# Performance work log

Hardware: AMD Instinct MI355X
Metric: run time of the kernel (lower is better)

## Reference

```python
import jax, jax.numpy as jnp
import numpy as np

DILATIONS_REST = (2, 4, 8, 16, 32, 64)


def _causal_conv(x, v, g, b, dilation):
    # weight-norm: w = g * v / ||v||_(in,k) per out-channel
    norm = jnp.sqrt(jnp.sum(v * v, axis=(1, 2), keepdims=True))
    w = g[:, None, None] * v / norm                      # [O, I, K]
    pad = (v.shape[2] - 1) * dilation                    # left-only causal pad
    y = jax.lax.conv_general_dilated(
        x, w, window_strides=(1,), padding=[(pad, 0)],
        rhs_dilation=(dilation,), dimension_numbers=('NCH', 'OIH', 'NCH'))
    return y + b[None, :, None]


def setup_inputs() -> dict:
    key = jax.random.key(0)
    ks = jax.random.split(key, 16)
    B, T, V, E = 64, 2048, 32000, 300
    inp = {
        'inputs': jax.random.randint(ks[0], (B, T), 0, V),
        'de_feature': jax.random.normal(ks[1], (B, 11), dtype=jnp.float32),
        'emb': jax.random.normal(ks[2], (V, E), dtype=jnp.float32) * 0.02,
        'v0': jax.random.normal(ks[3], (128, 300, 5), dtype=jnp.float32) * 0.05,
        'g0': jnp.ones((128,), dtype=jnp.float32),
        'b0': jax.random.normal(ks[4], (128,), dtype=jnp.float32) * 0.01,
        'vr': jax.random.normal(ks[5], (6, 128, 128, 5), dtype=jnp.float32) * 0.05,
        'gr': jnp.ones((6, 128), dtype=jnp.float32),
        'br': jax.random.normal(ks[6], (6, 128), dtype=jnp.float32) * 0.01,
        'fc1_w': jax.random.normal(ks[7], (64, 139), dtype=jnp.float32) * 0.08,
        'fc1_b': jnp.zeros((64,), dtype=jnp.float32),
        'fc2_w': jax.random.normal(ks[8], (32, 64), dtype=jnp.float32) * 0.12,
        'fc2_b': jnp.zeros((32,), dtype=jnp.float32),
        'fc3_w': jax.random.normal(ks[9], (1, 32), dtype=jnp.float32) * 0.17,
        'fc3_b': jnp.zeros((1,), dtype=jnp.float32),
    }
    return inp


def reference(inputs, de_feature, emb, v0, g0, b0, vr, gr, br,
              fc1_w, fc1_b, fc2_w, fc2_b, fc3_w, fc3_b):
    x = emb[inputs]                       # [B, T, 300]
    x = jnp.transpose(x, (0, 2, 1))       # [B, 300, T]
    x = jax.nn.relu(_causal_conv(x, v0, g0, b0, 1))
    for i, d in enumerate(DILATIONS_REST):
        x = jax.nn.relu(_causal_conv(x, vr[i], gr[i], br[i], d))
    emb_v = x[:, :, -1]                   # last timestep [B, 128]
    combo = jnp.concatenate([emb_v, de_feature], axis=1)  # [B, 139]
    h = jax.nn.relu(combo @ fc1_w.T + fc1_b)
    h = jax.nn.relu(h @ fc2_w.T + fc2_b)
    logits = h @ fc3_w.T + fc3_b          # [B, 1]
    return logits
```

## Files before the change

### kernel.cpp

```cpp
#include <hip/hip_runtime.h>


typedef __attribute__((ext_vector_type(8))) short bfrag8;
typedef __attribute__((ext_vector_type(4))) float floatx4;
typedef __attribute__((ext_vector_type(4))) short short4v;
typedef __attribute__((ext_vector_type(4))) float float4v;

__device__ __forceinline__ unsigned short f2bf(float f) {
  union { float f; unsigned u; } v; v.f = f;
  unsigned r = v.u + 0x7fffu + ((v.u >> 16) & 1u);
  return (unsigned short)(r >> 16);
}
__device__ __forceinline__ float bf2f(unsigned short h) {
  union { unsigned u; float f; } v; v.u = ((unsigned)h) << 16;
  return v.f;
}
__device__ __forceinline__ int swz(int row) { return ((row >> 1) & 7) << 4; }

__global__ __launch_bounds__(512)
void k_prep(const float* __restrict__ v0, const float* __restrict__ g0,
            const float* __restrict__ vr, const float* __restrict__ gr,
            const int* __restrict__ tokens, const float* __restrict__ emb,
            unsigned short* __restrict__ WB0, unsigned short* __restrict__ WBr,
            unsigned short* __restrict__ In0) {
  const int blk = blockIdx.x;
  if (blk >= 112) {
    const int gidx = ((blk - 112) << 9) + threadIdx.x;
    const int TOT = 64 * 520 * 80;
    for (int idx = gidx; idx < TOT; idx += 2560 * 512) {
      const int c8 = idx % 80;
      const int rem = idx / 80;
      const int p = rem % 520;
      const int b = rem / 520;
      short4v o = {0, 0, 0, 0};
      if (p < 509 && c8 < 75) {
        const int tok = tokens[(b << 11) + 1539 + p];
        const float4v v = *(const float4v*)(emb + (size_t)tok * 300 + (c8 << 2));
        o[0] = (short)f2bf(v[0]); o[1] = (short)f2bf(v[1]);
        o[2] = (short)f2bf(v[2]); o[3] = (short)f2bf(v[3]);
      }
      *(short4v*)(In0 + ((size_t)b * 520 + p) * 320 + (c8 << 2)) = o;
    }
    return;
  }
  const int gw = (blk << 3) + (threadIdx.x >> 6);
  const int lane = threadIdx.x & 63;
  if (gw < 128) {
    const int o = gw;
    const float* v = v0 + o * 1500;
    float ss = 0.f;
    for (int i = lane; i < 1500; i += 64) { const float x = v[i]; ss += x * x; }
#pragma unroll
    for (int off = 32; off; off >>= 1) ss += __shfl_xor(ss, off, 64);
    const float scale = g0[o] * rsqrtf(ss);
    const int ot = o >> 4;
    for (int kk = lane; kk < 1600; kk += 64) {
      const int tap = kk / 320, c = kk % 320;
      const float w = (c < 300) ? v[c * 5 + tap] * scale : 0.f;
      const int ks = kk >> 5;
      const int li = (o & 15) | (((kk >> 3) & 3) << 4);
      WB0[(((ot * 50 + ks) * 64 + li) << 3) | (kk & 7)] = f2bf(w);
    }
  } else {
    const int idx = gw - 128;
    const int l = idx >> 7, o = idx & 127;
    const float* v = vr + (size_t)(l * 128 + o) * 640;
    float ss = 0.f;
#pragma unroll
    for (int i = 0; i < 10; ++i) { const float x = v[lane + (i << 6)]; ss += x * x; }
#pragma unroll
    for (int off = 32; off; off >>= 1) ss += __shfl_xor(ss, off, 64);
    const float scale = gr[l * 128 + o] * rsqrtf(ss);
    unsigned short* WB = WBr + (size_t)l * 81920;
    const int ot = o >> 4;
#pragma unroll
    for (int i = 0; i < 10; ++i) {
      const int kk = lane + (i << 6);
      const int tap = kk >> 7, c = kk & 127;
      const float w = v[c * 5 + tap] * scale;
      const int ks = kk >> 5;
      const int li = (o & 15) | (((kk >> 3) & 3) << 4);
      WB[(((ot * 20 + ks) * 64 + li) << 3) | (kk & 7)] = f2bf(w);
    }
  }
}

__global__ __launch_bounds__(512, 1)
void k_conv0(const unsigned short* __restrict__ In0,
             const unsigned short* __restrict__ WB, const float* __restrict__ b0,
             unsigned short* __restrict__ A0) {
  __shared__ char buf[131 * 656];
  const int tid = threadIdx.x;
  const int qt = blockIdx.x, b = blockIdx.y;
  const char* src = (const char*)(In0 + ((size_t)b * 520 + (qt << 7)) * 320);
  for (int idx = tid; idx < 131 * 41; idx += 512) {
    const int r = idx / 41, s = idx - r * 41;
    float4v v = {0.f, 0.f, 0.f, 0.f};
    if (s < 40) v = *(const float4v*)(src + r * 640 + (s << 4));
    *(float4v*)(buf + r * 656 + (s << 4)) = v;
  }
  __syncthreads();
  const int lane = tid & 63, w = tid >> 6;
  const int og = w & 3, mg = w >> 2;
  const int qb = lane & 15, kg = lane >> 4;
  floatx4 acc[2][2];
#pragma unroll
  for (int m = 0; m < 2; ++m) {
    acc[m][0] = floatx4{0.f, 0.f, 0.f, 0.f};
    acc[m][1] = floatx4{0.f, 0.f, 0.f, 0.f};
  }
  const unsigned short* wb0 = WB + (size_t)((((og << 1) * 50) << 6) + lane) * 8;
#pragma unroll
  for (int tap = 0; tap < 5; ++tap) {
    bfrag8 bf0[10], bf1[10];
#pragma unroll
    for (int cs = 0; cs < 10; ++cs) {
      const int ks = tap * 10 + cs;
      bf0[cs] = *(const bfrag8*)(wb0 + (ks << 9));
      bf1[cs] = *(const bfrag8*)(wb0 + ((ks + 50) << 9));
    }
#pragma unroll
    for (int cs = 0; cs < 10; ++cs) {
      const int cb = (cs << 6) + (kg << 4);
#pragma unroll
      for (int m = 0; m < 2; ++m) {
        const int row = (((((mg << 1) + m) << 4) + qb) << 1) + tap;
        const bfrag8 a = *(const bfrag8*)(buf + row * 656 + cb);
        acc[m][0] = __builtin_amdgcn_mfma_f32_16x16x32_bf16(a, bf0[cs], acc[m][0], 0, 0, 0);
        acc[m][1] = __builtin_amdgcn_mfma_f32_16x16x32_bf16(a, bf1[cs], acc[m][1], 0, 0, 0);
      }
    }
  }
  unsigned short* ob = A0 + (((size_t)b << 8) + (qt << 6)) * 128;
  const int o0 = (og << 5) + qb;
  const float bv0 = b0[o0], bv1 = b0[o0 + 16];
#pragma unroll
  for (int m = 0; m < 2; ++m)
#pragma unroll
    for (int r = 0; r < 4; ++r) {
      const int ql = ((((mg << 1) + m) << 4) + (kg << 2)) + r;
      ob[ql * 128 + o0]      = f2bf(fmaxf(acc[m][0][r] + bv0, 0.f));
      ob[ql * 128 + o0 + 16] = f2bf(fmaxf(acc[m][1][r] + bv1, 0.f));
    }
}

template<int NMTW, int NOTW, int MTILES>
__device__ __forceinline__ void conv_rest(const char* bi, char* bo,
    const unsigned short* __restrict__ WBl, const float* __restrict__ bias,
    int w, int qb, int kg, int lane) {
  constexpr int NG = MTILES / NMTW;
  const int mg = (NG == 1) ? 0 : (w % NG);
  const int og = (NG == 1) ? w : (w / NG);
  if (og >= 8 / NOTW) return;
  floatx4 acc[NMTW][NOTW];
#pragma unroll
  for (int m = 0; m < NMTW; ++m)
#pragma unroll
    for (int j = 0; j < NOTW; ++j) acc[m][j] = floatx4{0.f, 0.f, 0.f, 0.f};
#pragma unroll
  for (int quarter = 0; quarter < 4; ++quarter) {
    bfrag8 bfs[NOTW][5];
#pragma unroll
    for (int j = 0; j < NOTW; ++j)
#pragma unroll
      for (int t = 0; t < 5; ++t)
        bfs[j][t] = *(const bfrag8*)(WBl +
            (size_t)(((((og * NOTW + j) * 20) + quarter * 5 + t) << 6) + lane) * 8);
#pragma unroll
    for (int t = 0; t < 5; ++t) {
      const int ks = quarter * 5 + t, tap = ks >> 2, cs = ks & 3;
#pragma unroll
      for (int m = 0; m < NMTW; ++m) {
        const int row = (((((mg * NMTW + m) << 4) + qb)) << 1) + tap;
        const int byte = ((row << 8) + (cs << 6) + (kg << 4)) ^ swz(row);
        const bfrag8 a = *(const bfrag8*)(bi + byte);
#pragma unroll
        for (int j = 0; j < NOTW; ++j)
          acc[m][j] = __builtin_amdgcn_mfma_f32_16x16x32_bf16(a, bfs[j][t], acc[m][j], 0, 0, 0);
      }
    }
  }
#pragma unroll
  for (int m = 0; m < NMTW; ++m)
#pragma unroll
    for (int j = 0; j < NOTW; ++j) {
      const int o = ((og * NOTW + j) << 4) + qb;
      const float bv = bias[o];
#pragma unroll
      for (int r = 0; r < 4; ++r) {
        const int qq = ((mg * NMTW + m) << 4) + (kg << 2) + r;
        const int byte2 = ((qq << 8) + (o << 1)) ^ swz(qq);
        *(unsigned short*)(bo + byte2) = f2bf(fmaxf(acc[m][j][r] + bv, 0.f));
      }
    }
}

__global__ __launch_bounds__(1024, 1)
void k_tail(const unsigned short* __restrict__ A0, const unsigned short* __restrict__ WBr,
            const float* __restrict__ br, const float* __restrict__ de,
            const float* __restrict__ w1, const float* __restrict__ b1,
            const float* __restrict__ w2, const float* __restrict__ b2,
            const float* __restrict__ w3, const float* __restrict__ b3,
            float* __restrict__ out) {
  __shared__ char lds[65024 + 32768 + 16384 + 384 + 2048];
  char* bufIn = lds;
  char* actP  = lds + 65024;
  char* actQ  = lds + 97792;
  float* h1   = (float*)(lds + 114176);
  float* h2   = (float*)(lds + 114432);
  const int tid = threadIdx.x, b = blockIdx.x;
  const int lane = tid & 63, w = tid >> 6;
  const int qb = lane & 15, kg = lane >> 4;

  const char* a0b = (const char*)(A0 + ((size_t)b << 15));
  for (int idx = tid; idx < 253 * 16; idx += 1024) {
    const int r = idx >> 4, s = idx & 15;
    *(float4v*)(bufIn + (((r << 8) + (s << 4)) ^ swz(r))) =
        *(const float4v*)(a0b + (r << 8) + (s << 4));
  }
  __syncthreads();

  conv_rest<2, 2, 8>(bufIn, actP, WBr + 0 * 81920, br + 0,   w, qb, kg, lane);
  __syncthreads();
  conv_rest<1, 2, 4>(actP, actQ, WBr + 1 * 81920, br + 128, w, qb, kg, lane);
  __syncthreads();
  conv_rest<1, 1, 2>(actQ, actP, WBr + 2 * 81920, br + 256, w, qb, kg, lane);
  __syncthreads();
  conv_rest<1, 1, 1>(actP, actQ, WBr + 3 * 81920, br + 384, w, qb, kg, lane);
  __syncthreads();
  conv_rest<1, 1, 1>(actQ, actP, WBr + 4 * 81920, br + 512, w, qb, kg, lane);
  __syncthreads();
  conv_rest<1, 1, 1>(actP, actQ, WBr + 5 * 81920, br + 640, w, qb, kg, lane);
  __syncthreads();

  const unsigned short* o6 = (const unsigned short*)actQ;
  if (tid < 512) {
    const int o1 = tid >> 3, part = tid & 7;
    const int j0 = part * 18;
    const int j1 = (j0 + 18 < 139) ? j0 + 18 : 139;
    float s = 0.f;
    const float* wrow = w1 + o1 * 139;
    for (int j = j0; j < j1; ++j) {
      const float x = (j < 128) ? bf2f(o6[j]) : de[b * 11 + (j - 128)];
      s += wrow[j] * x;
    }
    s += __shfl_down(s, 4, 64);
    s += __shfl_down(s, 2, 64);
    s += __shfl_down(s, 1, 64);
    if (part == 0) h1[o1] = fmaxf(s + b1[o1], 0.f);
  }
  __syncthreads();
  if (tid < 64) {
    const int o2 = tid >> 1, part = tid & 1;
    float s = 0.f;
    const float* wrow = w2 + o2 * 64 + part * 32;
    for (int j = 0; j < 32; ++j) s += wrow[j] * h1[part * 32 + j];
    s += __shfl_down(s, 1, 64);
    if (part == 0) h2[o2] = fmaxf(s + b2[o2], 0.f);
  }
  __syncthreads();
  if (tid < 32) {
    float s = w3[tid] * h2[tid];
    s += __shfl_down(s, 16, 64);
    s += __shfl_down(s, 8, 64);
    s += __shfl_down(s, 4, 64);
    s += __shfl_down(s, 2, 64);
    s += __shfl_down(s, 1, 64);
    if (tid == 0) out[b] = s + b3[0];
  }
}

extern "C" void kernel_launch(void* const* d_in, const int* in_sizes, int n_in,
                              void* d_out, int out_size, void* d_ws, size_t ws_size,
                              hipStream_t stream) {
  const int*   tokens = (const int*)  d_in[0];
  const float* de     = (const float*)d_in[1];
  const float* emb    = (const float*)d_in[2];
  const float* v0     = (const float*)d_in[3];
  const float* g0     = (const float*)d_in[4];
  const float* b0     = (const float*)d_in[5];
  const float* vr     = (const float*)d_in[6];
  const float* gr     = (const float*)d_in[7];
  const float* br     = (const float*)d_in[8];
  const float* w1     = (const float*)d_in[9];
  const float* b1     = (const float*)d_in[10];
  const float* w2     = (const float*)d_in[11];
  const float* b2     = (const float*)d_in[12];
  const float* w3     = (const float*)d_in[13];
  const float* b3     = (const float*)d_in[14];
  float* out = (float*)d_out;

  char* w = (char*)d_ws;
  unsigned short* WB0 = (unsigned short*)(w + 0);
  unsigned short* WBr = (unsigned short*)(w + 409600);
  unsigned short* In0 = (unsigned short*)(w + 1392640);
  unsigned short* A0  = (unsigned short*)(w + 22691840);

  hipLaunchKernelGGL(k_prep, dim3(112 + 2560), dim3(512), 0, stream,
                     v0, g0, vr, gr, tokens, emb, WB0, WBr, In0);
  hipLaunchKernelGGL(k_conv0, dim3(4, 64), dim3(512), 0, stream, In0, WB0, b0, A0);
  hipLaunchKernelGGL(k_tail, dim3(64), dim3(1024), 0, stream,
                     A0, WBr, br, de, w1, b1, w2, b2, w3, b3, out);
}
```

Measured before the change: 67.48 us.

## Fuse first causal conv into per-batch tail kernel, dropping intermediate buffer

The first dilated convolution now runs inside the per-batch network kernel. It loops over four time chunks staged in shared memory and writes its activations directly into the shared input buffer of the later layers. This removes a kernel launch and the global write/read of the layer-0 activations. The cost is less parallelism: conv0 now runs on only 64 blocks instead of 256, and shared memory is reused across stages.

```diff
diff --git a/kernel.cpp b/kernel.cpp
--- a/kernel.cpp
+++ b/kernel.cpp
@@ -85,65 +85,6 @@
   }
 }
 
-__global__ __launch_bounds__(512, 1)
-void k_conv0(const unsigned short* __restrict__ In0,
-             const unsigned short* __restrict__ WB, const float* __restrict__ b0,
-             unsigned short* __restrict__ A0) {
-  __shared__ char buf[131 * 656];
-  const int tid = threadIdx.x;
-  const int qt = blockIdx.x, b = blockIdx.y;
-  const char* src = (const char*)(In0 + ((size_t)b * 520 + (qt << 7)) * 320);
-  for (int idx = tid; idx < 131 * 41; idx += 512) {
-    const int r = idx / 41, s = idx - r * 41;
-    float4v v = {0.f, 0.f, 0.f, 0.f};
-    if (s < 40) v = *(const float4v*)(src + r * 640 + (s << 4));
-    *(float4v*)(buf + r * 656 + (s << 4)) = v;
-  }
-  __syncthreads();
-  const int lane = tid & 63, w = tid >> 6;
-  const int og = w & 3, mg = w >> 2;
-  const int qb = lane & 15, kg = lane >> 4;
-  floatx4 acc[2][2];
-#pragma unroll
-  for (int m = 0; m < 2; ++m) {
-    acc[m][0] = floatx4{0.f, 0.f, 0.f, 0.f};
-    acc[m][1] = floatx4{0.f, 0.f, 0.f, 0.f};
-  }
-  const unsigned short* wb0 = WB + (size_t)((((og << 1) * 50) << 6) + lane) * 8;
-#pragma unroll
-  for (int tap = 0; tap < 5; ++tap) {
-    bfrag8 bf0[10], bf1[10];
-#pragma unroll
-    for (int cs = 0; cs < 10; ++cs) {
-      const int ks = tap * 10 + cs;
-      bf0[cs] = *(const bfrag8*)(wb0 + (ks << 9));
-      bf1[cs] = *(const bfrag8*)(wb0 + ((ks + 50) << 9));
-    }
-#pragma unroll
-    for (int cs = 0; cs < 10; ++cs) {
-      const int cb = (cs << 6) + (kg << 4);
-#pragma unroll
-      for (int m = 0; m < 2; ++m) {
-        const int row = (((((mg << 1) + m) << 4) + qb) << 1) + tap;
-        const bfrag8 a = *(const bfrag8*)(buf + row * 656 + cb);
-        acc[m][0] = __builtin_amdgcn_mfma_f32_16x16x32_bf16(a, bf0[cs], acc[m][0], 0, 0, 0);
-        acc[m][1] = __builtin_amdgcn_mfma_f32_16x16x32_bf16(a, bf1[cs], acc[m][1], 0, 0, 0);
-      }
-    }
-  }
-  unsigned short* ob = A0 + (((size_t)b << 8) + (qt << 6)) * 128;
-  const int o0 = (og << 5) + qb;
-  const float bv0 = b0[o0], bv1 = b0[o0 + 16];
-#pragma unroll
-  for (int m = 0; m < 2; ++m)
-#pragma unroll
-    for (int r = 0; r < 4; ++r) {
-      const int ql = ((((mg << 1) + m) << 4) + (kg << 2)) + r;
-      ob[ql * 128 + o0]      = f2bf(fmaxf(acc[m][0][r] + bv0, 0.f));
-      ob[ql * 128 + o0 + 16] = f2bf(fmaxf(acc[m][1][r] + bv1, 0.f));
-    }
-}
-
 template<int NMTW, int NOTW, int MTILES>
 __device__ __forceinline__ void conv_rest(const char* bi, char* bo,
     const unsigned short* __restrict__ WBl, const float* __restrict__ bias,
@@ -196,29 +137,70 @@
 }
 
 __global__ __launch_bounds__(1024, 1)
-void k_tail(const unsigned short* __restrict__ A0, const unsigned short* __restrict__ WBr,
-            const float* __restrict__ br, const float* __restrict__ de,
-            const float* __restrict__ w1, const float* __restrict__ b1,
-            const float* __restrict__ w2, const float* __restrict__ b2,
-            const float* __restrict__ w3, const float* __restrict__ b3,
-            float* __restrict__ out) {
-  __shared__ char lds[65024 + 32768 + 16384 + 384 + 2048];
-  char* bufIn = lds;
-  char* actP  = lds + 65024;
-  char* actQ  = lds + 97792;
-  float* h1   = (float*)(lds + 114176);
-  float* h2   = (float*)(lds + 114432);
+void k_net(const unsigned short* __restrict__ In0,
+           const unsigned short* __restrict__ WB0, const unsigned short* __restrict__ WBr,
+           const float* __restrict__ b0, const float* __restrict__ br,
+           const float* __restrict__ de,
+           const float* __restrict__ w1, const float* __restrict__ b1,
+           const float* __restrict__ w2, const float* __restrict__ b2,
+           const float* __restrict__ w3, const float* __restrict__ b3,
+           float* __restrict__ out) {
+  __shared__ char lds[152880];
+  char* embChunk = lds;
+  char* actP = lds;
+  char* actQ = lds + 33536;
+  char* bufIn = lds + 85936;
+  float* h1 = (float*)(lds + 152496);
+  float* h2 = h1 + 64;
   const int tid = threadIdx.x, b = blockIdx.x;
   const int lane = tid & 63, w = tid >> 6;
   const int qb = lane & 15, kg = lane >> 4;
-
-  const char* a0b = (const char*)(A0 + ((size_t)b << 15));
-  for (int idx = tid; idx < 253 * 16; idx += 1024) {
-    const int r = idx >> 4, s = idx & 15;
-    *(float4v*)(bufIn + (((r << 8) + (s << 4)) ^ swz(r))) =
-        *(const float4v*)(a0b + (r << 8) + (s << 4));
-  }
-  __syncthreads();
+  const int og = w & 3, mg = w >> 2;
+
+  const unsigned short* wb0 = WB0 + (size_t)((((og << 1) * 50) << 6) + lane) * 8;
+  const int arow = ((mg << 4) + qb) << 1;
+  const int o0 = (og << 5) + qb;
+  const float bv0 = b0[o0], bv1 = b0[o0 + 16];
+  for (int qt = 0; qt < 4; ++qt) {
+    const char* src = (const char*)(In0 + ((size_t)b * 520 + (qt << 7)) * 320);
+    for (int idx = tid; idx < 131 * 41; idx += 1024) {
+      const int r = idx / 41, s = idx - r * 41;
+      float4v v = {0.f, 0.f, 0.f, 0.f};
+      if (s < 40) v = *(const float4v*)(src + r * 640 + (s << 4));
+      *(float4v*)(embChunk + r * 656 + (s << 4)) = v;
+    }
+    __syncthreads();
+    floatx4 acc0 = {0.f, 0.f, 0.f, 0.f}, acc1 = {0.f, 0.f, 0.f, 0.f};
+#pragma unroll
+    for (int tap = 0; tap < 5; ++tap) {
+#pragma unroll
+      for (int h = 0; h < 2; ++h) {
+        bfrag8 bf0[5], bf1[5];
+#pragma unroll
+        for (int j = 0; j < 5; ++j) {
+          const int ks = tap * 10 + h * 5 + j;
+          bf0[j] = *(const bfrag8*)(wb0 + (ks << 9));
+          bf1[j] = *(const bfrag8*)(wb0 + ((ks + 50) << 9));
+        }
+#pragma unroll
+        for (int j = 0; j < 5; ++j) {
+          const int cb = (((h * 5 + j) << 6)) + (kg << 4);
+          const bfrag8 a = *(const bfrag8*)(embChunk + (arow + tap) * 656 + cb);
+          acc0 = __builtin_amdgcn_mfma_f32_16x16x32_bf16(a, bf0[j], acc0, 0, 0, 0);
+          acc1 = __builtin_amdgcn_mfma_f32_16x16x32_bf16(a, bf1[j], acc1, 0, 0, 0);
+        }
+      }
+    }
+#pragma unroll
+    for (int r = 0; r < 4; ++r) {
+      const int qq = (qt << 6) + (mg << 4) + (kg << 2) + r;
+      *(unsigned short*)(bufIn + (((qq << 8) + (o0 << 1)) ^ swz(qq))) =
+          f2bf(fmaxf(acc0[r] + bv0, 0.f));
+      *(unsigned short*)(bufIn + (((qq << 8) + ((o0 + 16) << 1)) ^ swz(qq))) =
+          f2bf(fmaxf(acc1[r] + bv1, 0.f));
+    }
+    __syncthreads();
+  }
 
   conv_rest<2, 2, 8>(bufIn, actP, WBr + 0 * 81920, br + 0,   w, qb, kg, lane);
   __syncthreads();
@@ -294,11 +276,9 @@
   unsigned short* WB0 = (unsigned short*)(w + 0);
   unsigned short* WBr = (unsigned short*)(w + 409600);
   unsigned short* In0 = (unsigned short*)(w + 1392640);
-  unsigned short* A0  = (unsigned short*)(w + 22691840);
 
   hipLaunchKernelGGL(k_prep, dim3(112 + 2560), dim3(512), 0, stream,
                      v0, g0, vr, gr, tokens, emb, WB0, WBr, In0);
-  hipLaunchKernelGGL(k_conv0, dim3(4, 64), dim3(512), 0, stream, In0, WB0, b0, A0);
-  hipLaunchKernelGGL(k_tail, dim3(64), dim3(1024), 0, stream,
-                     A0, WBr, br, de, w1, b1, w2, b2, w3, b3, out);
-}
+  hipLaunchKernelGGL(k_net, dim3(64), dim3(1024), 0, stream,
+                     In0, WB0, WBr, b0, br, de, w1, b1, w2, b2, w3, b3, out);
+}
```

Measured after the change: 238.1 us. 253% more time.

## Split first dilated residual conv into its own wide-grid kernel before tail

Applied to the files above, without the earlier changes.

Moves the first residual conv layer (dilation 2) out of the per-batch 64-block tail kernel into a separate kernel launched on a 4x64 grid. The tail then processes only the remaining five layers, uses 512 threads and has a smaller LDS footprint. The aim is to spread the largest tail layer across more CUs instead of leaving it serialized in 64 blocks. In exchange it adds an extra launch and a global round trip for the intermediate activations. The MFMA inner loop is also reordered to iterate by tap and then channel slice.

```diff
diff --git a/kernel.cpp b/kernel.cpp
--- a/kernel.cpp
+++ b/kernel.cpp
@@ -144,13 +144,62 @@
     }
 }
 
+__global__ __launch_bounds__(512, 1)
+void k_conv1(const unsigned short* __restrict__ A0,
+             const unsigned short* __restrict__ WBr, const float* __restrict__ br,
+             unsigned short* __restrict__ L1out) {
+  __shared__ char abuf[68 * 256];
+  const int tid = threadIdx.x;
+  const int qt = blockIdx.x, b = blockIdx.y;
+  const char* a0b = (const char*)(A0 + ((size_t)b << 15));
+  for (int idx = tid; idx < 67 * 16; idx += 512) {
+    const int r = idx >> 4, s = idx & 15;
+    int rs = (qt << 6) + r; if (rs > 255) rs = 255;
+    *(float4v*)(abuf + (((r << 8) + (s << 4)) ^ swz(r))) =
+        *(const float4v*)(a0b + (rs << 8) + (s << 4));
+  }
+  __syncthreads();
+  const int lane = tid & 63, w = tid >> 6;
+  const int og = w & 3, mg = w >> 2;
+  const int qb = lane & 15, kg = lane >> 4;
+  floatx4 acc0 = {0.f, 0.f, 0.f, 0.f}, acc1 = {0.f, 0.f, 0.f, 0.f};
+  const unsigned short* wb = WBr + (size_t)((((og << 1) * 20) << 6) + lane) * 8;
+#pragma unroll
+  for (int tap = 0; tap < 5; ++tap) {
+    bfrag8 bf0[4], bf1[4];
+#pragma unroll
+    for (int cs = 0; cs < 4; ++cs) {
+      const int ks = (tap << 2) + cs;
+      bf0[cs] = *(const bfrag8*)(wb + (ks << 9));
+      bf1[cs] = *(const bfrag8*)(wb + ((ks + 20) << 9));
+    }
+#pragma unroll
+    for (int cs = 0; cs < 4; ++cs) {
+      const int cb = (cs << 6) + (kg << 4);
+      const int row = (((mg << 4) + qb) << 1) + tap;
+      const bfrag8 a = *(const bfrag8*)(abuf + (((row << 8) + cb) ^ swz(row)));
+      acc0 = __builtin_amdgcn_mfma_f32_16x16x32_bf16(a, bf0[cs], acc0, 0, 0, 0);
+      acc1 = __builtin_amdgcn_mfma_f32_16x16x32_bf16(a, bf1[cs], acc1, 0, 0, 0);
+    }
+  }
+  unsigned short* ob = L1out + (((size_t)b << 7) + (qt << 5)) * 128;
+  const int o0 = (og << 5) + qb;
+  const float bv0 = br[o0], bv1 = br[o0 + 16];
+#pragma unroll
+  for (int r = 0; r < 4; ++r) {
+    const int ql = (mg << 4) + (kg << 2) + r;
+    ob[ql * 128 + o0]      = f2bf(fmaxf(acc0[r] + bv0, 0.f));
+    ob[ql * 128 + o0 + 16] = f2bf(fmaxf(acc1[r] + bv1, 0.f));
+  }
+}
+
 template<int NMTW, int NOTW, int MTILES>
-__device__ __forceinline__ void conv_rest(const char* bi, char* bo,
+__device__ __forceinline__ void convT(const char* bi, char* bo,
     const unsigned short* __restrict__ WBl, const float* __restrict__ bias,
     int w, int qb, int kg, int lane) {
-  constexpr int NG = MTILES / NMTW;
-  const int mg = (NG == 1) ? 0 : (w % NG);
-  const int og = (NG == 1) ? w : (w / NG);
+  constexpr int NMG = MTILES / NMTW;
+  const int mg = (NMG == 1) ? 0 : (w % NMG);
+  const int og = (NMG == 1) ? w : (w / NMG);
   if (og >= 8 / NOTW) return;
   floatx4 acc[NMTW][NOTW];
 #pragma unroll
@@ -158,25 +207,24 @@
 #pragma unroll
     for (int j = 0; j < NOTW; ++j) acc[m][j] = floatx4{0.f, 0.f, 0.f, 0.f};
 #pragma unroll
-  for (int quarter = 0; quarter < 4; ++quarter) {
-    bfrag8 bfs[NOTW][5];
+  for (int tap = 0; tap < 5; ++tap) {
+    bfrag8 bfs[NOTW][4];
 #pragma unroll
     for (int j = 0; j < NOTW; ++j)
 #pragma unroll
-      for (int t = 0; t < 5; ++t)
-        bfs[j][t] = *(const bfrag8*)(WBl +
-            (size_t)(((((og * NOTW + j) * 20) + quarter * 5 + t) << 6) + lane) * 8);
-#pragma unroll
-    for (int t = 0; t < 5; ++t) {
-      const int ks = quarter * 5 + t, tap = ks >> 2, cs = ks & 3;
+      for (int cs = 0; cs < 4; ++cs)
+        bfs[j][cs] = *(const bfrag8*)(WBl +
+            (size_t)((((og * NOTW + j) * 20 + (tap << 2) + cs) << 6) + lane) * 8);
+#pragma unroll
+    for (int cs = 0; cs < 4; ++cs) {
+      const int cb = (cs << 6) + (kg << 4);
 #pragma unroll
       for (int m = 0; m < NMTW; ++m) {
-        const int row = (((((mg * NMTW + m) << 4) + qb)) << 1) + tap;
-        const int byte = ((row << 8) + (cs << 6) + (kg << 4)) ^ swz(row);
-        const bfrag8 a = *(const bfrag8*)(bi + byte);
+        const int row = (((mg * NMTW + m) << 4) + qb) * 2 + tap;
+        const bfrag8 a = *(const bfrag8*)(bi + (((row << 8) + cb) ^ swz(row)));
 #pragma unroll
         for (int j = 0; j < NOTW; ++j)
-          acc[m][j] = __builtin_amdgcn_mfma_f32_16x16x32_bf16(a, bfs[j][t], acc[m][j], 0, 0, 0);
+          acc[m][j] = __builtin_amdgcn_mfma_f32_16x16x32_bf16(a, bfs[j][cs], acc[m][j], 0, 0, 0);
       }
     }
   }
@@ -189,52 +237,54 @@
 #pragma unroll
       for (int r = 0; r < 4; ++r) {
         const int qq = ((mg * NMTW + m) << 4) + (kg << 2) + r;
-        const int byte2 = ((qq << 8) + (o << 1)) ^ swz(qq);
-        *(unsigned short*)(bo + byte2) = f2bf(fmaxf(acc[m][j][r] + bv, 0.f));
+        *(unsigned short*)(bo + (((qq << 8) + (o << 1)) ^ swz(qq))) =
+            f2bf(fmaxf(acc[m][j][r] + bv, 0.f));
       }
     }
 }
 
-__global__ __launch_bounds__(1024, 1)
-void k_tail(const unsigned short* __restrict__ A0, const unsigned short* __restrict__ WBr,
-            const float* __restrict__ br, const float* __restrict__ de,
-            const float* __restrict__ w1, const float* __restrict__ b1,
-            const float* __restrict__ w2, const float* __restrict__ b2,
-            const float* __restrict__ w3, const float* __restrict__ b3,
-            float* __restrict__ out) {
-  __shared__ char lds[65024 + 32768 + 16384 + 384 + 2048];
-  char* bufIn = lds;
-  char* actP  = lds + 65024;
-  char* actQ  = lds + 97792;
-  float* h1   = (float*)(lds + 114176);
-  float* h2   = (float*)(lds + 114432);
+__global__ __launch_bounds__(512, 1)
+void k_tail2(const unsigned short* __restrict__ L1out, const unsigned short* __restrict__ WBr,
+             const float* __restrict__ br, const float* __restrict__ de,
+             const float* __restrict__ w1, const float* __restrict__ b1,
+             const float* __restrict__ w2, const float* __restrict__ b2,
+             const float* __restrict__ w3, const float* __restrict__ b3,
+             float* __restrict__ out) {
+  __shared__ char lds[136 * 256 + 72 * 256 + 384];
+  char* bufA = lds;
+  char* bufB = lds + 136 * 256;
+  float* h1 = (float*)(lds + 136 * 256 + 72 * 256);
+  float* h2 = h1 + 64;
   const int tid = threadIdx.x, b = blockIdx.x;
   const int lane = tid & 63, w = tid >> 6;
   const int qb = lane & 15, kg = lane >> 4;
 
-  const char* a0b = (const char*)(A0 + ((size_t)b << 15));
-  for (int idx = tid; idx < 253 * 16; idx += 1024) {
+  const char* l1b = (const char*)(L1out + ((size_t)b << 14));
+  for (int idx = tid; idx < 136 * 16; idx += 512) {
     const int r = idx >> 4, s = idx & 15;
-    *(float4v*)(bufIn + (((r << 8) + (s << 4)) ^ swz(r))) =
-        *(const float4v*)(a0b + (r << 8) + (s << 4));
-  }
-  __syncthreads();
-
-  conv_rest<2, 2, 8>(bufIn, actP, WBr + 0 * 81920, br + 0,   w, qb, kg, lane);
-  __syncthreads();
-  conv_rest<1, 2, 4>(actP, actQ, WBr + 1 * 81920, br + 128, w, qb, kg, lane);
-  __syncthreads();
-  conv_rest<1, 1, 2>(actQ, actP, WBr + 2 * 81920, br + 256, w, qb, kg, lane);
-  __syncthreads();
-  conv_rest<1, 1, 1>(actP, actQ, WBr + 3 * 81920, br + 384, w, qb, kg, lane);
-  __syncthreads();
-  conv_rest<1, 1, 1>(actQ, actP, WBr + 4 * 81920, br + 512, w, qb, kg, lane);
-  __syncthreads();
-  conv_rest<1, 1, 1>(actP, actQ, WBr + 5 * 81920, br + 640, w, qb, kg, lane);
-  __syncthreads();
-
-  const unsigned short* o6 = (const unsigned short*)actQ;
-  if (tid < 512) {
+    float4v v = {0.f, 0.f, 0.f, 0.f};
+    if (r < 128) v = *(const float4v*)(l1b + (r << 8) + (s << 4));
+    *(float4v*)(bufA + (((r << 8) + (s << 4)) ^ swz(r))) = v;
+  }
+  for (int idx = tid; idx < 8 * 16; idx += 512) {
+    const int r = 64 + (idx >> 4), s = idx & 15;
+    *(float4v*)(bufB + (((r << 8) + (s << 4)) ^ swz(r))) = float4v{0.f, 0.f, 0.f, 0.f};
+  }
+  __syncthreads();
+
+  convT<2, 2, 4>(bufA, bufB, WBr + 1 * 81920, br + 128, w, qb, kg, lane);
+  __syncthreads();
+  convT<1, 2, 2>(bufB, bufA, WBr + 2 * 81920, br + 256, w, qb, kg, lane);
+  __syncthreads();
+  convT<1, 1, 1>(bufA, bufB, WBr + 3 * 81920, br + 384, w, qb, kg, lane);
+  __syncthreads();
+  convT<1, 1, 1>(bufB, bufA, WBr + 4 * 81920, br + 512, w, qb, kg, lane);
+  __syncthreads();
+  convT<1, 1, 1>(bufA, bufB, WBr + 5 * 81920, br + 640, w, qb, kg, lane);
+  __syncthreads();
+
+  const unsigned short* o6 = (const unsigned short*)bufB;
+  {
     const int o1 = tid >> 3, part = tid & 7;
     const int j0 = part * 18;
     const int j1 = (j0 + 18 < 139) ? j0 + 18 : 139;
@@ -291,14 +341,16 @@
   float* out = (float*)d_out;
 
   char* w = (char*)d_ws;
-  unsigned short* WB0 = (unsigned short*)(w + 0);
-  unsigned short* WBr = (unsigned short*)(w + 409600);
-  unsigned short* In0 = (unsigned short*)(w + 1392640);
-  unsigned short* A0  = (unsigned short*)(w + 22691840);
+  unsigned short* WB0   = (unsigned short*)(w + 0);
+  unsigned short* WBr   = (unsigned short*)(w + 409600);
+  unsigned short* In0   = (unsigned short*)(w + 1392640);
+  unsigned short* A0    = (unsigned short*)(w + 22691840);
+  unsigned short* L1out = (unsigned short*)(w + 26886144);
 
   hipLaunchKernelGGL(k_prep, dim3(112 + 2560), dim3(512), 0, stream,
                      v0, g0, vr, gr, tokens, emb, WB0, WBr, In0);
   hipLaunchKernelGGL(k_conv0, dim3(4, 64), dim3(512), 0, stream, In0, WB0, b0, A0);
-  hipLaunchKernelGGL(k_tail, dim3(64), dim3(1024), 0, stream,
-                     A0, WBr, br, de, w1, b1, w2, b2, w3, b3, out);
-}
+  hipLaunchKernelGGL(k_conv1, dim3(4, 64), dim3(512), 0, stream, A0, WBr, br, L1out);
+  hipLaunchKernelGGL(k_tail2, dim3(64), dim3(512), 0, stream,
+                     L1out, WBr, br, de, w1, b1, w2, b2, w3, b3, out);
+}
```

New measurement: 66.53 us. No clear change (-1.4%).
